# Performance work log

Hardware: AMD Instinct MI355X
Metric: run time of the kernel (lower is better)

The kernel has to match this reference:

```python
import jax, jax.numpy as jnp
import numpy as np


def setup_inputs() -> dict:
    key = jax.random.key(0)
    # batch of 1D signals; DST is applied along the last dimension
    x = jax.random.normal(key, (16384, 1024), dtype=jnp.float32)
    return {"x": x}


def reference(x):
    # DST-II: y_k = sum_{n=0}^{N-1} x_n * sin(pi/N * (n + 1/2) * (k + 1))
    # (The original docstring says 'cos' but the op is a discrete SINE transform;
    #  the DREAMPlace kernel computes the DST-II above via FFT-style tricks.)
    N = x.shape[-1]
    n = jnp.arange(N, dtype=x.dtype)
    k = jnp.arange(N, dtype=x.dtype)
    # [N, N] sine basis: rows indexed by n (input), cols by k (output)
    S = jnp.sin((jnp.pi / N) * (n[:, None] + 0.5) * (k[None, :] + 1.0))
    # batched transform over leading dims
    lead = x.shape[:-1]
    y = jnp.einsum('bn,nk->bk', x.reshape(-1, N), S)
    return y.reshape(*lead, N)
```

## Files before the change

kernel.cpp:

```cpp
#include <hip/hip_runtime.h>
#include <cstdint>


__device__ __forceinline__ float sinr(float r) {
  return __builtin_amdgcn_sinf(r);
}
__device__ __forceinline__ float cosr(float r) {
  float t = r + 0.25f;
  t -= (t >= 1.0f) ? 1.0f : 0.0f;
  return __builtin_amdgcn_sinf(t);
}

#define N_PT 1024
#define ROWS_PER_WAVE 2

__global__ __launch_bounds__(256) void dst_fft(const float* __restrict__ X,
                                               float* __restrict__ Y) {
  static constexpr int BR4[16] = {0, 8, 4, 12, 2, 10, 6, 14,
                                  1, 9, 5, 13, 3, 11, 7, 15};
  static constexpr float W16C[8] = {1.0f, 0.9238795325f, 0.7071067812f,
                                    0.3826834324f, 0.0f, -0.3826834324f,
                                    -0.7071067812f, -0.9238795325f};
  static constexpr float W16S[8] = {-0.0f, -0.3826834324f, -0.7071067812f,
                                    -0.9238795325f, -1.0f, -0.9238795325f,
                                    -0.7071067812f, -0.3826834324f};

  const int t = threadIdx.x;
  const int l = t & 63;
  const int wid = blockIdx.x * 4 + (t >> 6);
  const int h = __brev((unsigned)l) >> 26;

  float cS[6], sS[6];
#pragma unroll
  for (int st = 0; st < 6; ++st) {
    int H = 32 >> st;
    float r = (float)(l & (H - 1)) / (float)(2 * H);
    cS[st] = cosr(r);
    sS[st] = -sinr(r);
  }
  float gc[16], gs[16];
#pragma unroll
  for (int i = 0; i < 16; ++i) {
    float r = (float)(l * BR4[i]) * (1.0f / 1024.0f);
    gc[i] = cosr(r);
    gs[i] = -sinr(r);
  }
  float dc[16], dsn[16];
#pragma unroll
  for (int i = 0; i < 16; ++i) {
    float r = (float)(BR4[i] + 16 * h) * (1.0f / 4096.0f);
    dc[i] = cosr(r);
    dsn[i] = sinr(r);
  }

  for (int it = 0; it < ROWS_PER_WAVE; ++it) {
    const int row = wid * ROWS_PER_WAVE + it;
    const float* xr = X + (size_t)row * N_PT;

    float re[16], im[16], odd[8];
#pragma unroll
    for (int j = 0; j < 8; ++j) {
      float2 v = *(const float2*)(xr + 2 * l + 128 * j);
      re[j] = v.x;
      odd[j] = v.y;
    }
#pragma unroll
    for (int j = 0; j < 8; ++j)
      re[15 - j] = -__shfl_xor(odd[j], 63);
#pragma unroll
    for (int i = 0; i < 16; ++i) im[i] = 0.0f;

#pragma unroll
    for (int H = 8; H >= 1; H >>= 1) {
#pragma unroll
      for (int b = 0; b < 16; b += 2 * H) {
#pragma unroll
        for (int o = 0; o < H; ++o) {
          int i0 = b + o, i1 = i0 + H;
          float ar = re[i0] - re[i1], ai = im[i0] - im[i1];
          re[i0] += re[i1];
          im[i0] += im[i1];
          int tw = o * (8 / H);
          re[i1] = ar * W16C[tw] - ai * W16S[tw];
          im[i1] = ar * W16S[tw] + ai * W16C[tw];
        }
      }
    }

#pragma unroll
    for (int i = 0; i < 16; ++i) {
      float tr = re[i] * gc[i] - im[i] * gs[i];
      im[i] = re[i] * gs[i] + im[i] * gc[i];
      re[i] = tr;
    }

#pragma unroll
    for (int st = 0; st < 6; ++st) {
      const int H = 32 >> st;
      const bool up = (l & H) != 0;
      const float c = up ? cS[st] : 1.0f;
      const float s = up ? sS[st] : 0.0f;
      const float sg = up ? -1.0f : 1.0f;
#pragma unroll
      for (int i = 0; i < 16; ++i) {
        float tr = __shfl_xor(re[i], H);
        float ti = __shfl_xor(im[i], H);
        float ar = tr + sg * re[i];
        float ai = ti + sg * im[i];
        re[i] = ar * c - ai * s;
        im[i] = ar * s + ai * c;
      }
    }

    float cb[16];
#pragma unroll
    for (int i = 0; i < 16; ++i)
      cb[i] = re[i] * dc[i] + im[i] * dsn[i];

    float* yb = Y + (size_t)row * N_PT + (1008 - 16 * h);
#pragma unroll
    for (int g = 0; g < 4; ++g) {
      float4 o4;
      o4.x = cb[BR4[15 - (4 * g + 0)]];
      o4.y = cb[BR4[15 - (4 * g + 1)]];
      o4.z = cb[BR4[15 - (4 * g + 2)]];
      o4.w = cb[BR4[15 - (4 * g + 3)]];
      *(float4*)(yb + 4 * g) = o4;
    }
  }
}

extern "C" void kernel_launch(void* const* d_in, const int* in_sizes, int n_in,
                              void* d_out, int out_size, void* d_ws, size_t ws_size,
                              hipStream_t stream) {
  const float* X = (const float*)d_in[0];
  float* Y = (float*)d_out;
  dst_fft<<<dim3(2048), dim3(256), 0, stream>>>(X, Y);
}
```

Measured before the change: 137.7 us.

## Replace shuffle-based cross-lane FFT stages with LDS transpose and radix-16 pass

The six butterfly stages, each built from two cross-lane shuffles per element, are replaced by a swizzled LDS transpose, a second in-register radix-16 FFT with on-the-fly twiddles, and a final radix-4 step using shuffles. This is meant to cut the large number of DPP/ds_bpermute shuffle operations. In exchange it adds 8 KB of LDS per wave, computes more sin/cos per element in the output stage, and writes scalar strided stores instead of float4 vectors.

```diff
diff --git a/kernel.cpp b/kernel.cpp
--- a/kernel.cpp
+++ b/kernel.cpp
@@ -11,9 +11,6 @@
   return __builtin_amdgcn_sinf(t);
 }
 
-#define N_PT 1024
-#define ROWS_PER_WAVE 2
-
 __global__ __launch_bounds__(256) void dst_fft(const float* __restrict__ X,
                                                float* __restrict__ Y) {
   static constexpr int BR4[16] = {0, 8, 4, 12, 2, 10, 6, 14,
@@ -25,19 +22,21 @@
                                     -0.9238795325f, -1.0f, -0.9238795325f,
                                     -0.7071067812f, -0.3826834324f};
 
+  __shared__ __align__(16) float lds_all[4][64 * 32];
+
   const int t = threadIdx.x;
   const int l = t & 63;
-  const int wid = blockIdx.x * 4 + (t >> 6);
-  const int h = __brev((unsigned)l) >> 26;
+  const int w = t >> 6;
+  float* lds = &lds_all[w][0];
+  const int wid = blockIdx.x * 4 + w;
 
-  float cS[6], sS[6];
-#pragma unroll
-  for (int st = 0; st < 6; ++st) {
-    int H = 32 >> st;
-    float r = (float)(l & (H - 1)) / (float)(2 * H);
-    cS[st] = cosr(r);
-    sS[st] = -sinr(r);
-  }
+  const int c = l & 3;
+  const int m2l = l >> 2;
+  const int e = ((c & 1) << 1) | (c >> 1);
+  const int sstar = BR4[m2l];
+  const int chb = sstar >> 1;
+  const int subo = (sstar & 1) * 2;
+
   float gc[16], gs[16];
 #pragma unroll
   for (int i = 0; i < 16; ++i) {
@@ -45,17 +44,11 @@
     gc[i] = cosr(r);
     gs[i] = -sinr(r);
   }
-  float dc[16], dsn[16];
+
 #pragma unroll
-  for (int i = 0; i < 16; ++i) {
-    float r = (float)(BR4[i] + 16 * h) * (1.0f / 4096.0f);
-    dc[i] = cosr(r);
-    dsn[i] = sinr(r);
-  }
-
-  for (int it = 0; it < ROWS_PER_WAVE; ++it) {
-    const int row = wid * ROWS_PER_WAVE + it;
-    const float* xr = X + (size_t)row * N_PT;
+  for (int it = 0; it < 2; ++it) {
+    const int row = wid * 2 + it;
+    const float* xr = X + (size_t)row * 1024;
 
     float re[16], im[16], odd[8];
 #pragma unroll
@@ -86,7 +79,6 @@
         }
       }
     }
-
 #pragma unroll
     for (int i = 0; i < 16; ++i) {
       float tr = re[i] * gc[i] - im[i] * gs[i];
@@ -94,38 +86,73 @@
       re[i] = tr;
     }
 
+    __asm__ volatile("s_waitcnt lgkmcnt(0)" ::: "memory");
 #pragma unroll
-    for (int st = 0; st < 6; ++st) {
-      const int H = 32 >> st;
-      const bool up = (l & H) != 0;
-      const float c = up ? cS[st] : 1.0f;
-      const float s = up ? sS[st] : 0.0f;
-      const float sg = up ? -1.0f : 1.0f;
+    for (int ch = 0; ch < 8; ++ch) {
+      float4 v = make_float4(re[2 * ch], im[2 * ch],
+                             re[2 * ch + 1], im[2 * ch + 1]);
+      *(float4*)(lds + l * 32 + ((ch ^ (l & 7)) * 4)) = v;
+    }
+    __asm__ volatile("s_waitcnt lgkmcnt(0)" ::: "memory");
 #pragma unroll
-      for (int i = 0; i < 16; ++i) {
-        float tr = __shfl_xor(re[i], H);
-        float ti = __shfl_xor(im[i], H);
-        float ar = tr + sg * re[i];
-        float ai = ti + sg * im[i];
-        re[i] = ar * c - ai * s;
-        im[i] = ar * s + ai * c;
+    for (int i = 0; i < 16; ++i) {
+      int r = c + 4 * BR4[i];
+      int cp = chb ^ (r & 7);
+      float2 v = *(const float2*)(lds + r * 32 + cp * 4 + subo);
+      re[i] = v.x;
+      im[i] = v.y;
+    }
+
+#pragma unroll
+    for (int H = 1; H <= 8; H <<= 1) {
+#pragma unroll
+      for (int b = 0; b < 16; b += 2 * H) {
+#pragma unroll
+        for (int o = 0; o < H; ++o) {
+          int i0 = b + o, i1 = i0 + H;
+          int tw = o * (8 / H);
+          float tr = re[i1] * W16C[tw] - im[i1] * W16S[tw];
+          float ti = re[i1] * W16S[tw] + im[i1] * W16C[tw];
+          re[i1] = re[i0] - tr;
+          im[i1] = im[i0] - ti;
+          re[i0] += tr;
+          im[i0] += ti;
+        }
       }
     }
 
-    float cb[16];
 #pragma unroll
-    for (int i = 0; i < 16; ++i)
-      cb[i] = re[i] * dc[i] + im[i] * dsn[i];
+    for (int m = 0; m < 16; ++m) {
+      float r = (float)(c * m) * (1.0f / 64.0f);
+      float tc = cosr(r), ts = -sinr(r);
+      float tr = re[m] * tc - im[m] * ts;
+      im[m] = re[m] * ts + im[m] * tc;
+      re[m] = tr;
+    }
 
-    float* yb = Y + (size_t)row * N_PT + (1008 - 16 * h);
+    {
+      const float sgA = (c & 2) ? -1.0f : 1.0f;
+      const bool rot = (c == 3);
+      const float sgB = (c & 1) ? -1.0f : 1.0f;
 #pragma unroll
-    for (int g = 0; g < 4; ++g) {
-      float4 o4;
-      o4.x = cb[BR4[15 - (4 * g + 0)]];
-      o4.y = cb[BR4[15 - (4 * g + 1)]];
-      o4.z = cb[BR4[15 - (4 * g + 2)]];
-      o4.w = cb[BR4[15 - (4 * g + 3)]];
-      *(float4*)(yb + 4 * g) = o4;
+      for (int i = 0; i < 16; ++i) {
+        float tr = __shfl_xor(re[i], 2), ti = __shfl_xor(im[i], 2);
+        float ar = tr + sgA * re[i], ai = ti + sgA * im[i];
+        float br = rot ? ai : ar;
+        float bi = rot ? -ar : ai;
+        tr = __shfl_xor(br, 1);
+        ti = __shfl_xor(bi, 1);
+        re[i] = tr + sgB * br;
+        im[i] = ti + sgB * bi;
+      }
+    }
+
+    float* yr = Y + (size_t)row * 1024 + (1023 - m2l - 256 * e);
+#pragma unroll
+    for (int s2 = 0; s2 < 16; ++s2) {
+      int j = m2l + 16 * s2 + 256 * e;
+      float r = (float)j * (1.0f / 4096.0f);
+      yr[-16 * s2] = re[s2] * cosr(r) + im[s2] * sinr(r);
     }
   }
 }
```

Measured after the change: 118.9 us. 1.16x faster.
